# Kernel tuning notes

Measured on AMD Instinct MI355X. Metric: run time of the kernel, lower is better.

Reference implementation:

```python
import jax, jax.numpy as jnp
import numpy as np

NC = 32           # tessellation cells on [0,1]
N_POINTS = 2097152
EPS = 1e-10


def cpa_basis(nc):
    """Orthonormal (SVD) null-space basis of the CPA continuity constraints.
    Each cell c has velocity v(x) = a_c x + b_c; continuity at internal knots
    x_k = k/nc gives (nc-1) constraints on the 2*nc params -> basis (2nc, nc+1)."""
    L = np.zeros((nc - 1, 2 * nc))
    for k in range(1, nc):
        xk = k / nc
        L[k - 1, 2 * (k - 1)] = xk
        L[k - 1, 2 * (k - 1) + 1] = 1.0
        L[k - 1, 2 * k] = -xk
        L[k - 1, 2 * k + 1] = -1.0
    _, _, Vt = np.linalg.svd(L, full_matrices=True)
    return Vt[nc - 1:].T  # (2nc, nc+1)


B_NP = cpa_basis(NC)


def setup_inputs():
    key = jax.random.key(0)
    k1, k2 = jax.random.split(key)
    x = jax.random.uniform(k1, (N_POINTS,), dtype=jnp.float32)
    theta = 0.5 * jax.random.normal(k2, (1, NC + 1), dtype=jnp.float32)
    return {"x": x, "theta": theta}


def _transform(x, theta):
    """Closed-form CPAB integration: phi(x) = solution at t=1 of dphi/dt = v(phi),
    v piecewise affine. Within a cell the ODE has a closed form; a trajectory is
    monotone so it crosses each of the NC cells at most once -> scan of NC steps.
    Also accumulates log|dphi/dx| = integral of a(phi(s)) ds in closed form."""
    nc = NC
    h = 1.0 / nc
    A = (jnp.asarray(B_NP, x.dtype) @ theta[0]).reshape(nc, 2)  # per-cell (a, b)
    c0 = jnp.clip(jnp.floor(x * nc).astype(jnp.int32), 0, nc - 1)
    t0 = jnp.ones_like(x)      # remaining integration time
    lj0 = jnp.zeros_like(x)    # accumulated log-Jacobian

    def step(state, _):
        xs, t, c, lj = state
        a = A[c, 0]
        b = A[c, 1]
        v = a * xs + b
        # boundary in direction of motion (extreme cells extend to +/- inf)
        left = jnp.where(c == 0, -jnp.inf, c * h)
        right = jnp.where(c == nc - 1, jnp.inf, (c + 1) * h)
        xc = jnp.where(v > 0, right, left)
        finite = jnp.isfinite(xc)
        xcs = jnp.where(finite, xc, xs)
        big = jnp.abs(a) > EPS
        a_s = jnp.where(big, a, 1.0)
        # time to hit boundary: exp(a t) = v(xc)/v(x) (a != 0), (xc-x)/b (a == 0)
        vc = a * xcs + b
        r = vc / jnp.where(v == 0, 1.0, v)
        th_a = jnp.log(jnp.maximum(r, EPS)) / a_s
        th_b = (xcs - xs) / jnp.where(jnp.abs(b) > EPS, b, 1.0)
        t_hit = jnp.where(big, jnp.where(r > EPS, th_a, jnp.inf), th_b)
        valid = finite & (v != 0) & (t_hit > 0)
        t_hit = jnp.where(valid, t_hit, jnp.inf)
        cross = t_hit < t
        dt = jnp.where(cross, jnp.where(jnp.isfinite(t_hit), t_hit, 0.0), t)
        # closed-form in-cell flow psi(x, dt)
        psi = jnp.where(big, jnp.exp(a * dt) * (xs + b / a_s) - b / a_s, xs + b * dt)
        x_new = jnp.where(cross, xcs, psi)
        lj_new = lj + a * dt
        t_new = jnp.where(cross, t - dt, 0.0)
        c_new = jnp.clip(c + jnp.where(cross, jnp.where(v > 0, 1, -1), 0), 0, nc - 1)
        return (x_new, t_new, c_new, lj_new), None

    (z, _, _, lj), _ = jax.lax.scan(step, (x, t0, c0, lj0), None, length=nc)
    return z, lj


def reference(x, theta):
    z, log_dz_dx = _transform(x, theta)
    return (z, log_dz_dx)
```

## Files before the change

kernel.cpp:

```cpp
#include <hip/hip_runtime.h>
#include <math.h>

#define NCC  32
#define EPSF 1e-10f

struct MTab { float mt[33][64]; };

constexpr double csqrt_(double x) {
    double y = x > 1.0 ? x : 1.0;
    for (int i = 0; i < 80; ++i) y = 0.5 * (y + x / y);
    return y;
}

constexpr MTab make_mtab() {
    double Lm[31][64] = {};
    for (int k = 1; k < 32; ++k) {
        double xk = (double)k / 32.0;
        Lm[k - 1][2 * (k - 1)]     = xk;
        Lm[k - 1][2 * (k - 1) + 1] = 1.0;
        Lm[k - 1][2 * k]           = -xk;
        Lm[k - 1][2 * k + 1]       = -1.0;
    }
    double tau[31] = {};
    for (int i = 0; i < 31; ++i) {
        int E = 2 * i + 3; if (E > 63) E = 63;
        double xn2 = 0.0;
        for (int p = i + 1; p <= E; ++p) xn2 += Lm[i][p] * Lm[i][p];
        const double alpha = Lm[i][i];
        double tu = 0.0, sc = 0.0;
        if (xn2 != 0.0) {
            const double nrm  = csqrt_(alpha * alpha + xn2);
            const double beta = (alpha >= 0.0) ? -nrm : nrm;
            tu = (beta - alpha) / beta;
            sc = 1.0 / (alpha - beta);
        }
        for (int p = i + 1; p <= E; ++p) Lm[i][p] *= sc;
        Lm[i][i] = 1.0;
        tau[i] = tu;
        for (int j = i + 1; j < 31; ++j) {
            double s = 0.0;
            for (int p = i; p <= E; ++p) s += Lm[i][p] * Lm[j][p];
            s *= tu;
            for (int p = i; p <= E; ++p) Lm[j][p] -= s * Lm[i][p];
        }
    }
    MTab o{};
    for (int col = 0; col < 33; ++col) {
        double u[64] = {};
        u[31 + col] = 1.0;
        for (int i = 30; i >= 0; --i) {
            int E = 2 * i + 3; if (E > 63) E = 63;
            double s = 0.0;
            for (int p = i; p <= E; ++p) s += Lm[i][p] * u[p];
            s *= tau[i];
            for (int p = i; p <= E; ++p) u[p] -= s * Lm[i][p];
        }
        for (int p = 0; p < 64; ++p) o.mt[col][p] = (float)u[p];
    }
    return o;
}

__constant__ const MTab dM = make_mtab();

__global__ __launch_bounds__(256) void cpab_flow(const float* __restrict__ x_in,
                                                 const float* __restrict__ theta,
                                                 float* __restrict__ out, int n) {
    __shared__ float  sA[64];
    __shared__ float  aS[NCC], bS[NCC], boaS[NCC], vLS[NCC], vRS[NCC];
    __shared__ float2 TAP[2][NCC + 8];

    const int   tid = threadIdx.x;
    const float INF = __builtin_inff();

    if (tid < 64) {
        float acc = 0.0f;
#pragma unroll
        for (int j = 0; j < 33; ++j) acc = fmaf(dM.mt[j][tid], theta[j], acc);
        sA[tid] = acc;
    }
    __syncthreads();
    if (tid < NCC) {
        const float a   = sA[2 * tid];
        const float b   = sA[2 * tid + 1];
        const bool  big = fabsf(a) > EPSF;
        aS[tid]   = a;
        bS[tid]   = b;
        boaS[tid] = b / (big ? a : 1.0f);
        vLS[tid]  = __fadd_rn(__fmul_rn(a, __fmul_rn((float)tid,       0.03125f)), b);
        vRS[tid]  = __fadd_rn(__fmul_rn(a, __fmul_rn((float)(tid + 1), 0.03125f)), b);
    }
    __syncthreads();
    if (tid < 2 * (NCC + 8)) {
        const int   dd = tid / (NCC + 8);
        const int   j  = tid % (NCC + 8);
        float2 val = make_float2(INF, 0.0f);
        if (j >= 4 && j < NCC + 4) {
            const int   c     = j - 4;
            const float a     = aS[c];
            const float b     = bS[c];
            const float entry = __fmul_rn((float)(c + (dd ? 0 : 1)), 0.03125f);
            const float v     = dd ? vLS[c] : vRS[c];
            const bool  dirA  = v > 0.0f;
            const bool  fin   = dirA ? (c < NCC - 1) : (c > 0);
            const float xb    = __fmul_rn((float)(c + (dirA ? 1 : 0)), 0.03125f);
            const float xcs   = fin ? xb : entry;
            const float vc    = fin ? (dirA ? vRS[c] : vLS[c]) : v;
            const bool  v0    = (v == 0.0f);
            const float r     = vc / (v0 ? 1.0f : v);
            const bool  big   = fabsf(a) > EPSF;
            const float a_s   = big ? a : 1.0f;
            const float th_a  = logf(fmaxf(r, EPSF)) / a_s;
            const float bb    = (fabsf(b) > EPSF) ? b : 1.0f;
            const float th_b  = __fsub_rn(xcs, entry) / bb;
            float t_hit = big ? ((r > EPSF) ? th_a : INF) : th_b;
            const bool valid = fin && !v0 && (t_hit > 0.0f);
            t_hit = valid ? t_hit : INF;
            val = make_float2(t_hit, __fmul_rn(a, t_hit));
        }
        TAP[dd][j] = val;
    }
    __syncthreads();

    const int base = (blockIdx.x * blockDim.x + tid) << 2;
    if (base >= n) return;

    const float4 xv = *reinterpret_cast<const float4*>(x_in + base);
    float4 zo, jo;

#pragma unroll
    for (int q = 0; q < 4; ++q) {
        const float x0 = (q == 0) ? xv.x : (q == 1) ? xv.y : (q == 2) ? xv.z : xv.w;
        int c = (int)floorf(__fmul_rn(x0, 32.0f));
        c = min(max(c, 0), NCC - 1);

        float a = aS[c], b = bS[c];
        const float v    = __fadd_rn(__fmul_rn(a, x0), b);
        const bool  dirA = v > 0.0f;
        const bool  fin  = dirA ? (c < NCC - 1) : (c > 0);
        const float xb   = __fmul_rn((float)(c + (dirA ? 1 : 0)), 0.03125f);
        const float xcs  = fin ? xb : x0;
        const float vc   = fin ? (dirA ? vRS[c] : vLS[c]) : v;
        const bool  v0   = (v == 0.0f);
        const float r    = vc / (v0 ? 1.0f : v);
        const bool  big  = fabsf(a) > EPSF;
        const float a_s  = big ? a : 1.0f;
        const float th_a = logf(fmaxf(r, EPSF)) / a_s;
        float th_b = 0.0f;
        if (__any(!big)) {
            const float bb = (fabsf(b) > EPSF) ? b : 1.0f;
            th_b = __fsub_rn(xcs, x0) / bb;
        }
        float th = big ? ((r > EPSF) ? th_a : INF) : th_b;
        const bool valid = fin && !v0 && (th > 0.0f);
        th = valid ? th : INF;

        float t = 1.0f, lj = 0.0f;
        const bool cross0 = th < t;
        const int  d      = dirA ? 1 : -1;
        if (cross0) {
            t  = __fsub_rn(t, th);
            lj = __fmul_rn(a, th);
            c += d;
        }

        const float2* TAd = TAP[dirA ? 1 : 0] + 4;
        bool active = cross0;
        while (__any(active)) {
            if (active) {
                const float2 A1 = TAd[c];
                const float2 A2 = TAd[c + d];
                const bool  x1  = A1.x < t;
                const float t1  = __fsub_rn(t, A1.x);
                const float l1  = __fadd_rn(lj, A1.y);
                const bool  x2  = x1 && (A2.x < t1);
                t  = x2 ? __fsub_rn(t1, A2.x) : (x1 ? t1 : t);
                lj = x2 ? __fadd_rn(l1, A2.y) : (x1 ? l1 : lj);
                c += x2 ? 2 * d : (x1 ? d : 0);
                active = x2;
            }
        }

        const float xs = cross0 ? __fmul_rn((float)(c + (dirA ? 0 : 1)), 0.03125f)
                                : x0;
        a = aS[c]; b = bS[c];
        const bool  bigf = fabsf(a) > EPSF;
        const float boa  = boaS[c];
        const float ad   = __fmul_rn(a, t);
        const float ea   = expf(ad);
        const float psi  = bigf ? __fsub_rn(__fmul_rn(ea, __fadd_rn(xs, boa)), boa)
                                : __fadd_rn(xs, __fmul_rn(b, t));
        const float ljo  = __fadd_rn(lj, ad);
        if (q == 0) { zo.x = psi; jo.x = ljo; }
        if (q == 1) { zo.y = psi; jo.y = ljo; }
        if (q == 2) { zo.z = psi; jo.z = ljo; }
        if (q == 3) { zo.w = psi; jo.w = ljo; }
    }

    *reinterpret_cast<float4*>(out + base)     = zo;
    *reinterpret_cast<float4*>(out + n + base) = jo;
}

extern "C" void kernel_launch(void* const* d_in, const int* in_sizes, int n_in,
                              void* d_out, int out_size, void* d_ws, size_t ws_size,
                              hipStream_t stream) {
    (void)d_ws; (void)ws_size; (void)n_in; (void)out_size;
    const float* x     = (const float*)d_in[0];
    const float* theta = (const float*)d_in[1];
    float*       out   = (float*)d_out;
    const int    n     = in_sizes[0];

    const int threads = (n + 3) / 4;
    const int blocks  = (threads + 255) / 256;
    cpab_flow<<<blocks, 256, 0, stream>>>(x, theta, out, n);
}
```

Baseline: 19.01 us.

## Replace per-point cell-crossing loop with prefix-sum tables and binary search

Each block now builds per-start-cell, per-direction prefix tables of cumulative crossing times (a running max) and log-Jacobian sums. Each point then finds its final cell with a fixed 6-step binary search instead of a divergent while loop that walks cells two at a time. This removes warp divergence and the variable trip count, at the cost of a longer serial table build per block (64 threads doing 32 iterations each). The block size also rises to 512, and scalar paths are added for tails that are not a multiple of 4.

```diff
diff --git a/kernel.cpp b/kernel.cpp
--- a/kernel.cpp
+++ b/kernel.cpp
@@ -3,6 +3,7 @@
 
 #define NCC  32
 #define EPSF 1e-10f
+#define TPB  512
 
 struct MTab { float mt[33][64]; };
 
@@ -62,12 +63,15 @@
 
 __constant__ const MTab dM = make_mtab();
 
-__global__ __launch_bounds__(256) void cpab_flow(const float* __restrict__ x_in,
+__global__ __launch_bounds__(TPB) void cpab_flow(const float* __restrict__ x_in,
                                                  const float* __restrict__ theta,
                                                  float* __restrict__ out, int n) {
-    __shared__ float  sA[64];
-    __shared__ float  aS[NCC], bS[NCC], boaS[NCC], vLS[NCC], vRS[NCC];
-    __shared__ float2 TAP[2][NCC + 8];
+    __shared__ float sA[64];
+    __shared__ float aS[NCC], bS[NCC], boaS[NCC], vLS[NCC], vRS[NCC];
+    __shared__ float thf[2][NCC], ljf[2][NCC];
+    __shared__ float Up[2 * NCC][33];
+    __shared__ float Sa[2 * NCC][33];
+    __shared__ float La[2 * NCC][33];
 
     const int   tid = threadIdx.x;
     const float INF = __builtin_inff();
@@ -90,56 +94,88 @@
         vRS[tid]  = __fadd_rn(__fmul_rn(a, __fmul_rn((float)(tid + 1), 0.03125f)), b);
     }
     __syncthreads();
-    if (tid < 2 * (NCC + 8)) {
-        const int   dd = tid / (NCC + 8);
-        const int   j  = tid % (NCC + 8);
-        float2 val = make_float2(INF, 0.0f);
-        if (j >= 4 && j < NCC + 4) {
-            const int   c     = j - 4;
-            const float a     = aS[c];
-            const float b     = bS[c];
-            const float entry = __fmul_rn((float)(c + (dd ? 0 : 1)), 0.03125f);
-            const float v     = dd ? vLS[c] : vRS[c];
-            const bool  dirA  = v > 0.0f;
-            const bool  fin   = dirA ? (c < NCC - 1) : (c > 0);
-            const float xb    = __fmul_rn((float)(c + (dirA ? 1 : 0)), 0.03125f);
-            const float xcs   = fin ? xb : entry;
-            const float vc    = fin ? (dirA ? vRS[c] : vLS[c]) : v;
-            const bool  v0    = (v == 0.0f);
-            const float r     = vc / (v0 ? 1.0f : v);
-            const bool  big   = fabsf(a) > EPSF;
-            const float a_s   = big ? a : 1.0f;
-            const float th_a  = logf(fmaxf(r, EPSF)) / a_s;
-            const float bb    = (fabsf(b) > EPSF) ? b : 1.0f;
-            const float th_b  = __fsub_rn(xcs, entry) / bb;
-            float t_hit = big ? ((r > EPSF) ? th_a : INF) : th_b;
-            const bool valid = fin && !v0 && (t_hit > 0.0f);
-            t_hit = valid ? t_hit : INF;
-            val = make_float2(t_hit, __fmul_rn(a, t_hit));
-        }
-        TAP[dd][j] = val;
-    }
-    __syncthreads();
-
-    const int base = (blockIdx.x * blockDim.x + tid) << 2;
+    if (tid < 2 * NCC) {
+        const int   c     = tid & 31;
+        const int   dd    = tid >> 5;
+        const float a     = aS[c];
+        const float b     = bS[c];
+        const float entry = __fmul_rn((float)(c + (dd ? 0 : 1)), 0.03125f);
+        const float v     = dd ? vLS[c] : vRS[c];
+        const bool  dirA  = v > 0.0f;
+        const bool  fin   = dirA ? (c < NCC - 1) : (c > 0);
+        const float xb    = __fmul_rn((float)(c + (dirA ? 1 : 0)), 0.03125f);
+        const float xcs   = fin ? xb : entry;
+        const float vc    = fin ? (dirA ? vRS[c] : vLS[c]) : v;
+        const bool  v0    = (v == 0.0f);
+        const float r     = vc / (v0 ? 1.0f : v);
+        const bool  big   = fabsf(a) > EPSF;
+        const float a_s   = big ? a : 1.0f;
+        const float th_a  = logf(fmaxf(r, EPSF)) / a_s;
+        const float bb    = (fabsf(b) > EPSF) ? b : 1.0f;
+        const float th_b  = __fsub_rn(xcs, entry) / bb;
+        float t_hit = big ? ((r > EPSF) ? th_a : INF) : th_b;
+        const bool valid = fin && !v0 && (t_hit > 0.0f);
+        t_hit = valid ? t_hit : INF;
+        thf[dd][c] = t_hit;
+        ljf[dd][c] = __fmul_rn(a, t_hit);
+    }
+    __syncthreads();
+    if (tid < 2 * NCC) {
+        const int d  = tid >> 5;
+        const int c1 = tid & 31;
+        const int dh = d ? 1 : -1;
+        float S = 0.0f, LJ = 0.0f, Um = -INF;
+        Sa[tid][0] = 0.0f;
+        La[tid][0] = 0.0f;
+        for (int k = 1; k <= 32; ++k) {
+            const int cell = c1 + (k - 1) * dh;
+            float th = 4.0f, lp = 0.0f;
+            if (cell >= 0 && cell < NCC) {
+                th = thf[d][cell];
+                lp = ljf[d][cell];
+                if (!(th <= 2.0f)) { th = 4.0f; lp = 0.0f; }
+            }
+            const float U = __fadd_rn(S, th);
+            Um = fmaxf(Um, U);
+            S  = U;
+            LJ = __fadd_rn(LJ, lp);
+            Up[tid][k] = Um;
+            Sa[tid][k] = S;
+            La[tid][k] = LJ;
+        }
+    }
+    __syncthreads();
+
+    const int ti   = blockIdx.x * blockDim.x + tid;
+    const int base = ti << 2;
     if (base >= n) return;
-
-    const float4 xv = *reinterpret_cast<const float4*>(x_in + base);
+    const bool full = (base + 3 < n);
+
+    float4 xv;
+    if (full) {
+        xv = *reinterpret_cast<const float4*>(x_in + base);
+    } else {
+        xv.x = x_in[base];
+        xv.y = (base + 1 < n) ? x_in[base + 1] : 0.0f;
+        xv.z = (base + 2 < n) ? x_in[base + 2] : 0.0f;
+        xv.w = 0.0f;
+    }
     float4 zo, jo;
 
 #pragma unroll
     for (int q = 0; q < 4; ++q) {
         const float x0 = (q == 0) ? xv.x : (q == 1) ? xv.y : (q == 2) ? xv.z : xv.w;
-        int c = (int)floorf(__fmul_rn(x0, 32.0f));
-        c = min(max(c, 0), NCC - 1);
-
-        float a = aS[c], b = bS[c];
+        int c0 = (int)floorf(__fmul_rn(x0, 32.0f));
+        c0 = min(max(c0, 0), NCC - 1);
+
+        const float a    = aS[c0];
+        const float b    = bS[c0];
         const float v    = __fadd_rn(__fmul_rn(a, x0), b);
         const bool  dirA = v > 0.0f;
-        const bool  fin  = dirA ? (c < NCC - 1) : (c > 0);
-        const float xb   = __fmul_rn((float)(c + (dirA ? 1 : 0)), 0.03125f);
+        const bool  fin  = dirA ? (c0 < NCC - 1) : (c0 > 0);
+        const float xb   = __fmul_rn((float)(c0 + (dirA ? 1 : 0)), 0.03125f);
         const float xcs  = fin ? xb : x0;
-        const float vc   = fin ? (dirA ? vRS[c] : vLS[c]) : v;
+        const float vc   = fin ? (dirA ? vRS[c0] : vLS[c0]) : v;
         const bool  v0   = (v == 0.0f);
         const float r    = vc / (v0 ? 1.0f : v);
         const bool  big  = fabsf(a) > EPSF;
@@ -154,41 +190,40 @@
         const bool valid = fin && !v0 && (th > 0.0f);
         th = valid ? th : INF;
 
-        float t = 1.0f, lj = 0.0f;
-        const bool cross0 = th < t;
-        const int  d      = dirA ? 1 : -1;
-        if (cross0) {
-            t  = __fsub_rn(t, th);
-            lj = __fmul_rn(a, th);
-            c += d;
-        }
-
-        const float2* TAd = TAP[dirA ? 1 : 0] + 4;
-        bool active = cross0;
-        while (__any(active)) {
-            if (active) {
-                const float2 A1 = TAd[c];
-                const float2 A2 = TAd[c + d];
-                const bool  x1  = A1.x < t;
-                const float t1  = __fsub_rn(t, A1.x);
-                const float l1  = __fadd_rn(lj, A1.y);
-                const bool  x2  = x1 && (A2.x < t1);
-                t  = x2 ? __fsub_rn(t1, A2.x) : (x1 ? t1 : t);
-                lj = x2 ? __fadd_rn(l1, A2.y) : (x1 ? l1 : lj);
-                c += x2 ? 2 * d : (x1 ? d : 0);
-                active = x2;
-            }
-        }
-
-        const float xs = cross0 ? __fmul_rn((float)(c + (dirA ? 0 : 1)), 0.03125f)
+        const bool  cross0 = th < 1.0f;
+        const float t0     = __fsub_rn(1.0f, th);
+        const float lj0    = __fmul_rn(a, th);
+        const int   dh     = dirA ? 1 : -1;
+        const int   c1     = c0 + dh;
+        const int   c1c    = min(max(c1, 0), NCC - 1);
+        const int   row    = (dirA ? NCC : 0) + c1c;
+
+        int m = 0;
+#pragma unroll
+        for (int s = 32; s >= 1; s >>= 1) {
+            const int   cand  = m + s;
+            const int   candc = min(cand, 32);
+            const float u     = Up[row][candc];
+            m = ((cand <= 32) && (t0 > u)) ? cand : m;
+        }
+        const float Sm = Sa[row][m];
+        const float Lm = La[row][m];
+
+        const float t  = cross0 ? __fsub_rn(t0, Sm) : 1.0f;
+        const float lj = cross0 ? __fadd_rn(lj0, Lm) : 0.0f;
+        int cf = cross0 ? (c1 + m * dh) : c0;
+        cf = min(max(cf, 0), NCC - 1);
+        const float xs = cross0 ? __fmul_rn((float)(cf + (dirA ? 0 : 1)), 0.03125f)
                                 : x0;
-        a = aS[c]; b = bS[c];
-        const bool  bigf = fabsf(a) > EPSF;
-        const float boa  = boaS[c];
-        const float ad   = __fmul_rn(a, t);
+
+        const float af   = aS[cf];
+        const float bf   = bS[cf];
+        const bool  bigf = fabsf(af) > EPSF;
+        const float boa  = boaS[cf];
+        const float ad   = __fmul_rn(af, t);
         const float ea   = expf(ad);
         const float psi  = bigf ? __fsub_rn(__fmul_rn(ea, __fadd_rn(xs, boa)), boa)
-                                : __fadd_rn(xs, __fmul_rn(b, t));
+                                : __fadd_rn(xs, __fmul_rn(bf, t));
         const float ljo  = __fadd_rn(lj, ad);
         if (q == 0) { zo.x = psi; jo.x = ljo; }
         if (q == 1) { zo.y = psi; jo.y = ljo; }
@@ -196,8 +231,14 @@
         if (q == 3) { zo.w = psi; jo.w = ljo; }
     }
 
-    *reinterpret_cast<float4*>(out + base)     = zo;
-    *reinterpret_cast<float4*>(out + n + base) = jo;
+    if (full) {
+        *reinterpret_cast<float4*>(out + base)     = zo;
+        *reinterpret_cast<float4*>(out + n + base) = jo;
+    } else {
+        out[base] = zo.x;             out[n + base] = jo.x;
+        if (base + 1 < n) { out[base + 1] = zo.y; out[n + base + 1] = jo.y; }
+        if (base + 2 < n) { out[base + 2] = zo.z; out[n + base + 2] = jo.z; }
+    }
 }
 
 extern "C" void kernel_launch(void* const* d_in, const int* in_sizes, int n_in,
@@ -209,7 +250,7 @@
     float*       out   = (float*)d_out;
     const int    n     = in_sizes[0];
 
-    const int threads = (n + 3) / 4;
-    const int blocks  = (threads + 255) / 256;
-    cpab_flow<<<blocks, 256, 0, stream>>>(x, theta, out, n);
-}
+    const int threads4 = (n + 3) >> 2;
+    const int blocks   = (threads4 + TPB - 1) / TPB;
+    cpab_flow<<<blocks, TPB, 0, stream>>>(x, theta, out, n);
+}
```

Measured after the change: 20.06 us. 1.06x slower.
